# Optimization experiments

Measured on AMD Instinct MI355X. Metric: run time of the kernel, lower is better.

Reference implementation:

```python
import jax, jax.numpy as jnp
import numpy as np

MIN_LEN = 4      # g.min_word_length
MAX_LEN = 10     # g.max_word_length
THRESH = 0.05    # g.init_threshold
NEG = -1e9


def setup_inputs() -> dict:
    key = jax.random.key(0)
    ks = jax.random.split(key, 6)
    B, L, F, D, U, V = 16, 64, 60, 256, 600, 10000
    x = jax.random.normal(ks[0], (B, L, F), jnp.float32)            # batch dense feat matrix
    unit_feats = jax.random.normal(ks[1], (U, F), jnp.float32)      # per-unit features
    W = jax.random.normal(ks[2], (F, D), jnp.float32) * 0.1         # FeatEmbedding weight
    lengths = jax.random.randint(ks[3], (B,), MIN_LEN, L + 1)       # sentence lengths
    indexed_segments = jax.random.randint(ks[4], (V, MAX_LEN), 0, U)  # vocab -> unit ids
    vocab_length = jax.random.randint(ks[5], (V,), MIN_LEN, MAX_LEN + 1)
    return dict(x=x, unit_feats=unit_feats, W=W, lengths=lengths,
                indexed_segments=indexed_segments, vocab_length=vocab_length)


def reference(x, unit_feats, W, lengths, indexed_segments, vocab_length):
    B, L, _ = x.shape
    V, J = indexed_segments.shape
    # embedding: features -> char_emb space
    word_repr = x @ W                 # [B, L, D]
    unit_repr = unit_feats @ W        # [U, D]
    # cosine similarity between every segment position and every unit
    wn = word_repr / (jnp.linalg.norm(word_repr, axis=-1, keepdims=True) + 1e-8)
    un = unit_repr / (jnp.linalg.norm(unit_repr, axis=-1, keepdims=True) + 1e-8)
    sim = jnp.einsum('bld,ud->blu', wn, un)  # [B, L, U]
    # pad so span gathers past the end read zeros (masked later by `viable`)
    sim_pad = jnp.pad(sim, ((0, 0), (0, J), (0, 0)))
    # accumulate per-position unit scores along each vocab word's unit sequence
    acc = jnp.zeros((B, L, V), sim.dtype)
    per_len = []
    for j in range(J):  # fixed small loop over word-length positions
        # sim at start+j for unit indexed_segments[v, j] -> [B, L, V]
        s_j = sim_pad[:, j:j + L, :][:, :, indexed_segments[:, j]]
        acc = acc + s_j
        if j + 1 >= MIN_LEN:
            per_len.append(acc / (j + 1))  # length-normalized match score
    scores = jnp.stack(per_len, axis=2)  # [B, len_s=L, len_e=E, V]
    E = scores.shape[2]
    k = jnp.arange(E) + MIN_LEN                          # candidate word lengths
    ends = jnp.arange(L)[:, None] + k[None, :] - 1        # [L, E]
    viable = ends[None] < lengths[:, None, None]          # [B, L, E]
    len_match = vocab_length[None, None, None, :] == k[None, None, :, None]
    mask = viable[..., None] & len_match                  # [B, L, E, V]
    masked = jnp.where(mask, scores, NEG)
    # best vocab word per span candidate
    value = masked.max(axis=-1)                           # [B, L, E]
    matched_vocab = masked.argmax(axis=-1)                # [B, L, E]
    matched = value > THRESH
    # best span candidate per batch element (eval path: hard max)
    flat = value.reshape(B, -1)                           # [B, L*E]
    best_inds = flat.argmax(axis=-1)
    best_scores = flat.max(axis=-1)
    best_starts = best_inds // E
    best_ends = best_inds % E + best_starts + MIN_LEN - 1
    any_matched = matched.reshape(B, -1).any(axis=-1)
    best_vocab = jnp.take_along_axis(matched_vocab.reshape(B, -1), best_inds[:, None], axis=1)[:, 0]
    return best_scores, best_starts, best_ends, any_matched, best_vocab
```

## Files before the change

### kernel.cpp

```cpp
#include <hip/hip_runtime.h>
#include <math.h>

#define BB 16
#define LL 64
#define FF 60
#define DD 256
#define UU 600
#define VV 10000
#define JMAX 10
#define MINL 4
#define EE 7
#define NEG (-1e9f)
#define TH 0.05f
#define BCAP 10240

#define UNT_OFF   0
#define WNT_OFF   163840
#define SIM_OFF   425984
#define CNT_OFF   1040384
#define SRT_OFF   1040392
#define VAL_OFF   1613832
#define VOC_OFF   1628168

__global__ __launch_bounds__(256) void k_prep(const int* __restrict__ seg,
                                              const int* __restrict__ vlen,
                                              const float* __restrict__ x,
                                              const float* __restrict__ uf,
                                              const float* __restrict__ W,
                                              unsigned int* __restrict__ cnt,
                                              unsigned int* __restrict__ srt,
                                              float* __restrict__ unT,
                                              float* __restrict__ wnT) {
    __shared__ unsigned long long sP[4][2];
    __shared__ int wTab[4][8];
    __shared__ int sBase[8];
    int blk = blockIdx.x;
    if (blk < 40) {
        int tid  = threadIdx.x;
        int lane = tid & 63;
        int w    = tid >> 6;
        int v    = blk * 256 + tid;

        unsigned long long p0 = 0, p1 = 0;
        int lim = blk * 256;
        for (int i = tid; i < lim; i += 256) {
            int e2 = vlen[i] - MINL;
            if (e2 < 4) p0 += 1ull << (e2 * 16);
            else        p1 += 1ull << ((e2 - 4) * 16);
        }
#pragma unroll
        for (int m = 32; m > 0; m >>= 1) {
            p0 += __shfl_xor(p0, m, 64);
            p1 += __shfl_xor(p1, m, 64);
        }
        if (lane == 0) { sP[w][0] = p0; sP[w][1] = p1; }

        int e = (v < VV) ? (vlen[v] - MINL) : -1;
        unsigned long long below = (lane == 0) ? 0ull : (~0ull >> (64 - lane));
        unsigned long long mym = 0;
#pragma unroll
        for (int b2 = 0; b2 < EE; ++b2) {
            unsigned long long m = __ballot(e == b2);
            if (lane == 0) wTab[w][b2] = (int)__popcll(m);
            if (e == b2) mym = m;
        }
        __syncthreads();
        if (tid < EE) {
            unsigned long long q0 = sP[0][0] + sP[1][0] + sP[2][0] + sP[3][0];
            unsigned long long q1 = sP[0][1] + sP[1][1] + sP[2][1] + sP[3][1];
            int base = (tid < 4) ? (int)((q0 >> (tid * 16)) & 0xffffull)
                                 : (int)((q1 >> ((tid - 4) * 16)) & 0xffffull);
            sBase[tid] = base;
            if (blk == 39)
                cnt[tid] = (unsigned)(base + wTab[0][tid] + wTab[1][tid]
                                           + wTab[2][tid] + wTab[3][tid]);
        }
        __syncthreads();

        if (v < VV) {
            int prior = sBase[e];
#pragma unroll
            for (int w2 = 0; w2 < 4; ++w2) if (w2 < w) prior += wTab[w2][e];
            unsigned pos = (unsigned)(prior + (int)__popcll(mym & below));

            const int* s = seg + v * JMAX;
            unsigned int t[10];
#pragma unroll
            for (int j = 0; j < JMAX; ++j) t[j] = (unsigned int)(s[j] * 13 + j);
            unsigned int* dst = srt + ((size_t)e * BCAP + pos) * 8;
            uint4 qa, qb;
            qa.x = t[0] | (t[1] << 16);
            qa.y = t[2] | (t[3] << 16);
            qa.z = t[4] | (t[5] << 16);
            qa.w = t[6] | (t[7] << 16);
            qb.x = t[8] | (t[9] << 16);
            qb.y = (unsigned int)v;
            qb.z = 0; qb.w = 0;
            ((uint4*)dst)[0] = qa;
            ((uint4*)dst)[1] = qb;
        }
    } else {
        int w = threadIdx.x >> 6;
        int lane = threadIdx.x & 63;
        int id = (blk - 40) * 4 + w;
        const float* row;
        float* outB;
        int stride, col;
        if (id < UU) { row = uf + id * FF; outB = unT; stride = 640;  col = id; }
        else { int bl = id - UU; row = x + bl * FF; outB = wnT; stride = 1024; col = bl; }

        float r0 = 0.f, r1 = 0.f, r2 = 0.f, r3 = 0.f;
#pragma unroll 4
        for (int f = 0; f < FF; ++f) {
            float xv = row[f];
            r0 += xv * W[f * DD + lane];
            r1 += xv * W[f * DD + lane + 64];
            r2 += xv * W[f * DD + lane + 128];
            r3 += xv * W[f * DD + lane + 192];
        }
        float ss = r0 * r0 + r1 * r1 + r2 * r2 + r3 * r3;
#pragma unroll
        for (int m = 32; m > 0; m >>= 1) ss += __shfl_xor(ss, m, 64);
        float inv = 1.0f / (sqrtf(ss) + 1e-8f);
        outB[(lane      ) * stride + col] = r0 * inv;
        outB[(lane +  64) * stride + col] = r1 * inv;
        outB[(lane + 128) * stride + col] = r2 * inv;
        outB[(lane + 192) * stride + col] = r3 * inv;
    }
}

__global__ __launch_bounds__(320) void k_sim(const float* __restrict__ unT,
                                             const float* __restrict__ wnT,
                                             const int* __restrict__ lengths,
                                             float* __restrict__ sim) {
    int blk = blockIdx.x;
    int b  = blk >> 5;
    int r  = blk & 31;
    int l0 = (r >> 1) * 4;
    if (l0 >= lengths[b]) return;
    int uh = r & 1;
    int bl0 = b * 64 + l0;
    int u = uh * 320 + threadIdx.x;

    float a0 = 0.f, a1 = 0.f, a2 = 0.f, a3 = 0.f;
#pragma unroll 8
    for (int d = 0; d < DD; ++d) {
        float4 wv = *(const float4*)(wnT + d * 1024 + bl0);
        float v  = unT[d * 640 + u];
        a0 += wv.x * v;
        a1 += wv.y * v;
        a2 += wv.z * v;
        a3 += wv.w * v;
    }
    if (u < UU) {
        sim[(bl0 + 0) * UU + u] = a0;
        sim[(bl0 + 1) * UU + u] = a1;
        sim[(bl0 + 2) * UU + u] = a2;
        sim[(bl0 + 3) * UU + u] = a3;
    }
}

template<int K>
__device__ __forceinline__ void seg_pass4(const unsigned int* __restrict__ srt,
                                          const float* __restrict__ lds,
                                          int e, int r0, int r1, int lane, int wave,
                                          float (*redS)[8], int (*redV)[8]) {
    float s0 = -1e30f, s1 = -1e30f, s2 = -1e30f, s3 = -1e30f;
    int w0 = VV, w1 = VV, w2 = VV, w3 = VV;
    for (int p = r0 + lane; p < r1; p += 64) {
        const uint4* pp = (const uint4*)(srt + ((size_t)e * BCAP + p) * 8);
        uint4 qa = pp[0];
        uint4 qb = pp[1];
        unsigned int tw[5] = {qa.x, qa.y, qa.z, qa.w, qb.x};
        int v = (int)qb.y;
        float a0 = 0.f, a1 = 0.f, a2 = 0.f, a3 = 0.f;
#pragma unroll
        for (int j = 0; j < K; ++j) {
            int idx = (int)((tw[j >> 1] >> ((j & 1) * 16)) & 0xffffu);
            a0 += lds[idx];
            a1 += lds[idx + 1];
            a2 += lds[idx + 2];
            a3 += lds[idx + 3];
        }
        float n0 = a0 / (float)K;
        float n1 = a1 / (float)K;
        float n2 = a2 / (float)K;
        float n3 = a3 / (float)K;
        bool p0 = (n0 > s0) || (n0 == s0 && v < w0);
        bool p1 = (n1 > s1) || (n1 == s1 && v < w1);
        bool p2 = (n2 > s2) || (n2 == s2 && v < w2);
        bool p3 = (n3 > s3) || (n3 == s3 && v < w3);
        s0 = p0 ? n0 : s0;  w0 = p0 ? v : w0;
        s1 = p1 ? n1 : s1;  w1 = p1 ? v : w1;
        s2 = p2 ? n2 : s2;  w2 = p2 ? v : w2;
        s3 = p3 ? n3 : s3;  w3 = p3 ? v : w3;
    }
#pragma unroll
    for (int off = 32; off > 0; off >>= 1) {
        float os; int ov;
        os = __shfl_down(s0, off, 64); ov = __shfl_down(w0, off, 64);
        if (os > s0 || (os == s0 && ov < w0)) { s0 = os; w0 = ov; }
        os = __shfl_down(s1, off, 64); ov = __shfl_down(w1, off, 64);
        if (os > s1 || (os == s1 && ov < w1)) { s1 = os; w1 = ov; }
        os = __shfl_down(s2, off, 64); ov = __shfl_down(w2, off, 64);
        if (os > s2 || (os == s2 && ov < w2)) { s2 = os; w2 = ov; }
        os = __shfl_down(s3, off, 64); ov = __shfl_down(w3, off, 64);
        if (os > s3 || (os == s3 && ov < w3)) { s3 = os; w3 = ov; }
    }
    if (lane == 0) {
        redS[e * 4 + 0][wave] = s0; redV[e * 4 + 0][wave] = w0;
        redS[e * 4 + 1][wave] = s1; redV[e * 4 + 1][wave] = w1;
        redS[e * 4 + 2][wave] = s2; redV[e * 4 + 2][wave] = w2;
        redS[e * 4 + 3][wave] = s3; redV[e * 4 + 3][wave] = w3;
    }
}

__global__ __launch_bounds__(512, 8) void k_score(const float* __restrict__ sim,
                                                  const unsigned int* __restrict__ srt,
                                                  const unsigned int* __restrict__ cnt,
                                                  const int* __restrict__ lengths,
                                                  float* __restrict__ val,
                                                  int* __restrict__ voc) {
    __shared__ float lds[UU * 13];
    __shared__ float redS[28][8];
    __shared__ int   redV[28][8];

    int blk = blockIdx.x;
    int half = blk >> 8;
    int rest = blk & 255;
    int b  = rest >> 4;
    int l0 = (rest & 15) * 4;
    int tid = threadIdx.x;
    int len = lengths[b];

    if (l0 + MINL - 1 >= len) {
        if (tid < 28) {
            int e  = tid >> 2;
            int dl = tid & 3;
            int o = (half * BB * LL + b * 64 + l0 + dl) * EE + e;
            val[o] = NEG;
            voc[o] = 0;
        }
        return;
    }

    if (tid < 224) {
        redS[tid >> 3][tid & 7] = -1e30f;
        redV[tid >> 3][tid & 7] = VV;
    }
    for (int u = tid; u < UU; u += 512) {
#pragma unroll
        for (int r = 0; r < 13; ++r) {
            int m = l0 + r;
            lds[u * 13 + r] = (m < LL) ? sim[(b * 64 + m) * UU + u] : 0.0f;
        }
    }
    __syncthreads();

    int wave = tid >> 6, lane = tid & 63;

    unsigned nlo[EE], nhi[EE], Bw[EE];
    unsigned Wtot = 0;
#pragma unroll
    for (int e = 0; e < EE; ++e) {
        unsigned n = cnt[e];
        unsigned lo = half ? (n >> 1) : 0;
        unsigned hi = half ? n : (n >> 1);
        if (l0 + e + MINL - 1 >= len) { lo = 0; hi = 0; }
        nlo[e] = lo; nhi[e] = hi;
        Bw[e] = Wtot;
        Wtot += (hi - lo) * (unsigned)(e + MINL);
    }
    unsigned qlo = (unsigned)(((unsigned long long)Wtot * (unsigned)wave) >> 3);
    unsigned qhi = (unsigned)(((unsigned long long)Wtot * (unsigned)(wave + 1)) >> 3);

#pragma unroll
    for (int e = 0; e < EE; ++e) {
        unsigned K = (unsigned)(e + MINL);
        unsigned segw = (nhi[e] - nlo[e]) * K;
        unsigned Be = Bw[e];
        if (qhi <= Be || qlo >= Be + segw || segw == 0) continue;
        unsigned a = (qlo > Be) ? (qlo - Be) : 0;
        unsigned bb = qhi - Be; if (bb > segw) bb = segw;
        int r0 = (int)(nlo[e] + (a + K - 1) / K);
        int r1 = (int)(nlo[e] + (bb + K - 1) / K);
        if (r1 <= r0) continue;
        switch (e) {
            case 0: seg_pass4<4> (srt, lds, 0, r0, r1, lane, wave, redS, redV); break;
            case 1: seg_pass4<5> (srt, lds, 1, r0, r1, lane, wave, redS, redV); break;
            case 2: seg_pass4<6> (srt, lds, 2, r0, r1, lane, wave, redS, redV); break;
            case 3: seg_pass4<7> (srt, lds, 3, r0, r1, lane, wave, redS, redV); break;
            case 4: seg_pass4<8> (srt, lds, 4, r0, r1, lane, wave, redS, redV); break;
            case 5: seg_pass4<9> (srt, lds, 5, r0, r1, lane, wave, redS, redV); break;
            case 6: seg_pass4<10>(srt, lds, 6, r0, r1, lane, wave, redS, redV); break;
        }
    }
    __syncthreads();

    if (tid < 28) {
        int e  = tid >> 2;
        int dl = tid & 3;
        float s = redS[tid][0];
        int  vv = redV[tid][0];
#pragma unroll
        for (int w2 = 1; w2 < 8; ++w2) {
            float os = redS[tid][w2];
            int   ov = redV[tid][w2];
            if (os > s || (os == s && ov < vv)) { s = os; vv = ov; }
        }
        int lg = l0 + dl;
        int k = e + MINL;
        bool viable = (lg + k - 1) < len;
        int o = (half * BB * LL + b * 64 + lg) * EE + e;
        val[o] = viable ? s : NEG;
        voc[o] = viable ? vv : 0;
    }
}

__global__ __launch_bounds__(512) void k_final(const float* __restrict__ val,
                                               const int* __restrict__ voc,
                                               float* __restrict__ out) {
    __shared__ float sS[8];
    __shared__ int   sI[8];
    __shared__ int   sV[8];
    __shared__ int   sA[8];
    int b = blockIdx.x;
    int t = threadIdx.x;
    float s = -3e38f;
    int idx = 1 << 30;
    int vc = 0;
    int any = 0;
    if (t < LL * EE) {
        int o0 = b * LL * EE + t;
        int o1 = BB * LL * EE + o0;
        float s0 = val[o0], s1 = val[o1];
        int   v0 = voc[o0], v1 = voc[o1];
        bool sel = (s1 > s0) || (s1 == s0 && v1 < v0);
        s  = sel ? s1 : s0;
        vc = sel ? v1 : v0;
        idx = t;
        any = (s > TH) ? 1 : 0;
    }
#pragma unroll
    for (int off = 32; off > 0; off >>= 1) {
        float os = __shfl_down(s, off, 64);
        int   oi = __shfl_down(idx, off, 64);
        int   ov = __shfl_down(vc, off, 64);
        int   oa = __shfl_down(any, off, 64);
        if (os > s || (os == s && oi < idx)) { s = os; idx = oi; vc = ov; }
        any |= oa;
    }
    int w = t >> 6, lane = t & 63;
    if (lane == 0) { sS[w] = s; sI[w] = idx; sV[w] = vc; sA[w] = any; }
    __syncthreads();
    if (t == 0) {
        for (int w2 = 1; w2 < 8; ++w2) {
            float os = sS[w2];
            int   oi = sI[w2];
            if (os > s || (os == s && oi < idx)) { s = os; idx = oi; vc = sV[w2]; }
            any |= sA[w2];
        }
        int start = idx / EE;
        int e = idx - start * EE;
        int end = e + start + MINL - 1;
        out[b]      = s;
        out[16 + b] = (float)start;
        out[32 + b] = (float)end;
        out[48 + b] = any ? 1.0f : 0.0f;
        out[64 + b] = (float)vc;
    }
}

extern "C" void kernel_launch(void* const* d_in, const int* in_sizes, int n_in,
                              void* d_out, int out_size, void* d_ws, size_t ws_size,
                              hipStream_t stream) {
    const float* x       = (const float*)d_in[0];
    const float* uf      = (const float*)d_in[1];
    const float* W       = (const float*)d_in[2];
    const int*   lengths = (const int*)d_in[3];
    const int*   seg     = (const int*)d_in[4];
    const int*   vlen    = (const int*)d_in[5];
    float* out = (float*)d_out;
    float* ws  = (float*)d_ws;

    float*        unT = ws + UNT_OFF;
    float*        wnT = ws + WNT_OFF;
    float*        sim = ws + SIM_OFF;
    unsigned int* cnt = (unsigned int*)(ws + CNT_OFF);
    unsigned int* srt = (unsigned int*)(ws + SRT_OFF);
    float*        val = ws + VAL_OFF;
    int*          voc = (int*)(ws + VOC_OFF);

    k_prep<<<446, 256, 0, stream>>>(seg, vlen, x, uf, W, cnt, srt, unT, wnT);
    k_sim<<<512, 320, 0, stream>>>(unT, wnT, lengths, sim);
    k_score<<<512, 512, 0, stream>>>(sim, srt, cnt, lengths, val, voc);
    k_final<<<BB, 512, 0, stream>>>(val, voc, out);
}
```

Measured before the change: 155.7 us.

## Split vocab scoring across four block groups and unroll candidate loads by two

```diff
diff --git a/kernel.cpp b/kernel.cpp
--- a/kernel.cpp
+++ b/kernel.cpp
@@ -13,6 +13,7 @@
 #define NEG (-1e9f)
 #define TH 0.05f
 #define BCAP 10240
+#define NQ 4
 
 #define UNT_OFF   0
 #define WNT_OFF   163840
@@ -20,7 +21,7 @@
 #define CNT_OFF   1040384
 #define SRT_OFF   1040392
 #define VAL_OFF   1613832
-#define VOC_OFF   1628168
+#define VOC_OFF   1642504
 
 __global__ __launch_bounds__(256) void k_prep(const int* __restrict__ seg,
                                               const int* __restrict__ vlen,
@@ -167,10 +168,9 @@
                                           float (*redS)[8], int (*redV)[8]) {
     float s0 = -1e30f, s1 = -1e30f, s2 = -1e30f, s3 = -1e30f;
     int w0 = VV, w1 = VV, w2 = VV, w3 = VV;
-    for (int p = r0 + lane; p < r1; p += 64) {
-        const uint4* pp = (const uint4*)(srt + ((size_t)e * BCAP + p) * 8);
-        uint4 qa = pp[0];
-        uint4 qb = pp[1];
+    const unsigned int* base = srt + (size_t)e * BCAP * 8;
+
+    auto proc = [&](uint4 qa, uint4 qb) {
         unsigned int tw[5] = {qa.x, qa.y, qa.z, qa.w, qb.x};
         int v = (int)qb.y;
         float a0 = 0.f, a1 = 0.f, a2 = 0.f, a3 = 0.f;
@@ -182,18 +182,32 @@
             a2 += lds[idx + 2];
             a3 += lds[idx + 3];
         }
-        float n0 = a0 / (float)K;
-        float n1 = a1 / (float)K;
-        float n2 = a2 / (float)K;
-        float n3 = a3 / (float)K;
-        bool p0 = (n0 > s0) || (n0 == s0 && v < w0);
-        bool p1 = (n1 > s1) || (n1 == s1 && v < w1);
-        bool p2 = (n2 > s2) || (n2 == s2 && v < w2);
-        bool p3 = (n3 > s3) || (n3 == s3 && v < w3);
-        s0 = p0 ? n0 : s0;  w0 = p0 ? v : w0;
-        s1 = p1 ? n1 : s1;  w1 = p1 ? v : w1;
-        s2 = p2 ? n2 : s2;  w2 = p2 ? v : w2;
-        s3 = p3 ? n3 : s3;  w3 = p3 ? v : w3;
+        bool p0 = (a0 > s0) || (a0 == s0 && v < w0);
+        bool p1 = (a1 > s1) || (a1 == s1 && v < w1);
+        bool p2 = (a2 > s2) || (a2 == s2 && v < w2);
+        bool p3 = (a3 > s3) || (a3 == s3 && v < w3);
+        s0 = p0 ? a0 : s0;  w0 = p0 ? v : w0;
+        s1 = p1 ? a1 : s1;  w1 = p1 ? v : w1;
+        s2 = p2 ? a2 : s2;  w2 = p2 ? v : w2;
+        s3 = p3 ? a3 : s3;  w3 = p3 ? v : w3;
+    };
+
+    int p = r0 + lane;
+    for (; p + 64 < r1; p += 128) {
+        const uint4* ppA = (const uint4*)(base + (size_t)p * 8);
+        const uint4* ppB = (const uint4*)(base + (size_t)(p + 64) * 8);
+        uint4 qaA = ppA[0];
+        uint4 qbA = ppA[1];
+        uint4 qaB = ppB[0];
+        uint4 qbB = ppB[1];
+        proc(qaA, qbA);
+        proc(qaB, qbB);
+    }
+    if (p < r1) {
+        const uint4* pp = (const uint4*)(base + (size_t)p * 8);
+        uint4 qa = pp[0];
+        uint4 qb = pp[1];
+        proc(qa, qb);
     }
 #pragma unroll
     for (int off = 32; off > 0; off >>= 1) {
@@ -226,7 +240,7 @@
     __shared__ int   redV[28][8];
 
     int blk = blockIdx.x;
-    int half = blk >> 8;
+    int qtr  = blk >> 8;
     int rest = blk & 255;
     int b  = rest >> 4;
     int l0 = (rest & 15) * 4;
@@ -237,7 +251,7 @@
         if (tid < 28) {
             int e  = tid >> 2;
             int dl = tid & 3;
-            int o = (half * BB * LL + b * 64 + l0 + dl) * EE + e;
+            int o = (qtr * BB * LL + b * 64 + l0 + dl) * EE + e;
             val[o] = NEG;
             voc[o] = 0;
         }
@@ -264,8 +278,8 @@
 #pragma unroll
     for (int e = 0; e < EE; ++e) {
         unsigned n = cnt[e];
-        unsigned lo = half ? (n >> 1) : 0;
-        unsigned hi = half ? n : (n >> 1);
+        unsigned lo = (n * (unsigned)qtr) / NQ;
+        unsigned hi = (n * (unsigned)(qtr + 1)) / NQ;
         if (l0 + e + MINL - 1 >= len) { lo = 0; hi = 0; }
         nlo[e] = lo; nhi[e] = hi;
         Bw[e] = Wtot;
@@ -311,8 +325,9 @@
         int lg = l0 + dl;
         int k = e + MINL;
         bool viable = (lg + k - 1) < len;
-        int o = (half * BB * LL + b * 64 + lg) * EE + e;
-        val[o] = viable ? s : NEG;
+        float sn = s / (float)k;
+        int o = (qtr * BB * LL + b * 64 + lg) * EE + e;
+        val[o] = viable ? sn : NEG;
         voc[o] = viable ? vv : 0;
     }
 }
@@ -332,12 +347,15 @@
     int any = 0;
     if (t < LL * EE) {
         int o0 = b * LL * EE + t;
-        int o1 = BB * LL * EE + o0;
-        float s0 = val[o0], s1 = val[o1];
-        int   v0 = voc[o0], v1 = voc[o1];
-        bool sel = (s1 > s0) || (s1 == s0 && v1 < v0);
-        s  = sel ? s1 : s0;
-        vc = sel ? v1 : v0;
+        s  = val[o0];
+        vc = voc[o0];
+#pragma unroll
+        for (int q = 1; q < NQ; ++q) {
+            int oq = q * BB * LL * EE + o0;
+            float sq = val[oq];
+            int   vq = voc[oq];
+            if (sq > s || (sq == s && vq < vc)) { s = sq; vc = vq; }
+        }
         idx = t;
         any = (s > TH) ? 1 : 0;
     }
@@ -393,6 +411,6 @@
 
     k_prep<<<446, 256, 0, stream>>>(seg, vlen, x, uf, W, cnt, srt, unT, wnT);
     k_sim<<<512, 320, 0, stream>>>(unT, wnT, lengths, sim);
-    k_score<<<512, 512, 0, stream>>>(sim, srt, cnt, lengths, val, voc);
+    k_score<<<NQ * 256, 512, 0, stream>>>(sim, srt, cnt, lengths, val, voc);
     k_final<<<BB, 512, 0, stream>>>(val, voc, out);
 }
```

After: 164.3 us. +5.5%, slower.
